# Optimization experiments

Hardware: AMD Instinct MI355X
Metric: run time of the kernel (lower is better)

Reference implementation:

```python
import jax, jax.numpy as jnp
import numpy as np

D_MODEL = 1024
NUM_HEADS = 16
D_K = D_MODEL // NUM_HEADS
THETA = 10000.0
SEQ = 4096
BATCH = 1


def _rope(x, token_positions):
    # x: [b, h, s, d_k]; interleaved even/odd rotation as in the torch module
    kd = jnp.arange(0, D_K, 2, dtype=jnp.float32) / D_K          # [d_k/2]
    angles = token_positions[:, None].astype(jnp.float32) / (THETA ** kd)  # [s, d_k/2]
    cos_pos = jnp.cos(angles)
    sin_pos = jnp.sin(angles)
    x_even = x[..., 0::2]
    x_odd = x[..., 1::2]
    rot_even = x_even * cos_pos - x_odd * sin_pos
    rot_odd = x_even * sin_pos + x_odd * cos_pos
    rot = jnp.stack([rot_even, rot_odd], axis=-1)                # [..., d_k/2, 2]
    return rot.reshape(*x.shape[:-1], D_K)


def setup_inputs() -> dict:
    key = jax.random.key(0)
    k1, k2, k3 = jax.random.split(key, 3)
    std_qkv = np.sqrt(2.0 / (D_MODEL + 3 * D_MODEL))
    std_o = np.sqrt(2.0 / (D_MODEL + D_MODEL))
    x = jax.random.normal(k1, (BATCH, SEQ, D_MODEL), dtype=jnp.float32)
    Wqkv = jax.random.normal(k2, (3 * D_MODEL, D_MODEL), dtype=jnp.float32) * std_qkv
    Wo = jax.random.normal(k3, (D_MODEL, D_MODEL), dtype=jnp.float32) * std_o
    token_positions = jnp.arange(SEQ, dtype=jnp.int32)
    return {"x": x, "Wqkv": Wqkv, "Wo": Wo, "token_positions": token_positions}


def reference(x, Wqkv, Wo, token_positions):
    b, s, _ = x.shape
    qkv = jnp.einsum('bsd,ed->bse', x, Wqkv)                      # [b, s, 3*d_model]
    q, k, v = jnp.split(qkv, 3, axis=-1)

    def to_heads(t):
        return t.reshape(b, s, NUM_HEADS, D_K).transpose(0, 2, 1, 3)  # [b, h, s, d_k]

    q, k, v = to_heads(q), to_heads(k), to_heads(v)
    q = _rope(q, token_positions)
    k = _rope(k, token_positions)

    scores = jnp.einsum('bhqd,bhkd->bhqk', q, k) / jnp.sqrt(jnp.float32(D_K))
    mask = jnp.tril(jnp.ones((s, s), dtype=bool))
    scores = jnp.where(mask, scores, -jnp.inf)
    attn = jax.nn.softmax(scores, axis=-1)
    out = jnp.einsum('bhqk,bhkd->bhqd', attn, v)                  # [b, h, s, d_k]
    out = out.transpose(0, 2, 1, 3).reshape(b, s, D_MODEL)
    return jnp.einsum('bsd,ed->bse', out, Wo)
```

## Files before the change

kernel.cpp:

```cpp
#include <hip/hip_runtime.h>
#include <cstdint>

typedef unsigned short u16;
typedef __attribute__((ext_vector_type(8))) short short8;
typedef __attribute__((ext_vector_type(4))) float float4v;

__device__ __forceinline__ float bf2f(u16 u) {
    union { unsigned int i; float f; } v; v.i = ((unsigned int)u) << 16; return v.f;
}
__device__ __forceinline__ u16 f2bf(float f) {
    union { float f; unsigned int i; } v; v.f = f;
    unsigned int i = v.i;
    i += 0x7fffu + ((i >> 16) & 1u);
    return (u16)(i >> 16);
}
__device__ __forceinline__ unsigned cvt_pk_bf16(float lo, float hi) {
    unsigned r;
    asm("v_cvt_pk_bf16_f32 %0, %1, %2" : "=v"(r) : "v"(lo), "v"(hi));
    return r;
}
__device__ __forceinline__ void gl2lds16(const u16* g, u16* l) {
    __builtin_amdgcn_global_load_lds((const __attribute__((address_space(1))) void*)g,
                                     (__attribute__((address_space(3))) void*)l, 16, 0, 0);
}
__device__ __forceinline__ uint4 cvt8(const float* __restrict__ p) {
    float4 a = *(const float4*)p;
    float4 b = *(const float4*)(p + 4);
    u16 t[8] = {f2bf(a.x), f2bf(a.y), f2bf(a.z), f2bf(a.w),
                f2bf(b.x), f2bf(b.y), f2bf(b.z), f2bf(b.w)};
    return *(const uint4*)t;
}

__global__ void cvt_xw(const float* __restrict__ x, const float* __restrict__ wq,
                       const int* __restrict__ pos,
                       u16* __restrict__ xb, u16* __restrict__ wqb,
                       float2* __restrict__ tb) {
    int i = blockIdx.x * blockDim.x + threadIdx.x;
    if (i < 524288) {
        *(uint4*)(xb + (size_t)i * 8) = cvt8(x + (size_t)i * 8);
    } else if (i < 917504) {
        int j = i - 524288;
        *(uint4*)(wqb + (size_t)j * 8) = cvt8(wq + (size_t)j * 8);
    } else {
        int j = i - 917504;
        int s = j >> 5, f = j & 31;
        float freq = __expf(-(float)f * 0.2878231366242557f);
        float ang  = (float)pos[s] * freq;
        float sn, cs;
        __sincosf(ang, &sn, &cs);
        float2 t; t.x = cs; t.y = sn;
        tb[j] = t;
    }
}

__global__ __launch_bounds__(256) void gemm_qkv(const u16* __restrict__ A,
                                                const u16* __restrict__ B,
                                                u16* __restrict__ C,
                                                const float2* __restrict__ tb) {
    __shared__ u16 As[128 * 32];
    __shared__ u16 Bs[128 * 32];
    const int tid  = threadIdx.x;
    const int wave = tid >> 6, lane = tid & 63;
    const int lg = lane >> 4, lr = lane & 15;
    const int bm = blockIdx.x * 128, bn = blockIdx.y * 128;
    const int wm = (wave & 1) * 64, wn = (wave >> 1) * 64;
    const int row = tid >> 2, co = (tid & 3) * 8;

    float4v acc[4][4] = {};

    for (int k0 = 0; k0 < 1024; k0 += 32) {
        gl2lds16(A + (size_t)(bm + row) * 1024 + k0 + co,      As + tid * 8);
        gl2lds16(A + (size_t)(bm + 64 + row) * 1024 + k0 + co, As + (tid + 256) * 8);
        gl2lds16(B + (size_t)(bn + row) * 1024 + k0 + co,      Bs + tid * 8);
        gl2lds16(B + (size_t)(bn + 64 + row) * 1024 + k0 + co, Bs + (tid + 256) * 8);
        __syncthreads();

        short8 af[4], bf[4];
        #pragma unroll
        for (int i = 0; i < 4; ++i)
            af[i] = *(const short8*)(As + (wm + i * 16 + lr) * 32 + lg * 8);
        #pragma unroll
        for (int j = 0; j < 4; ++j)
            bf[j] = *(const short8*)(Bs + (wn + j * 16 + lr) * 32 + lg * 8);
        #pragma unroll
        for (int i = 0; i < 4; ++i)
            #pragma unroll
            for (int j = 0; j < 4; ++j)
                acc[i][j] = __builtin_amdgcn_mfma_f32_16x16x32_bf16(af[i], bf[j], acc[i][j], 0, 0, 0);
        __syncthreads();
    }

    const int colbase = bn + wn;
    const bool dorope = colbase < 2048;
    const float qsc = (colbase < 1024) ? 0.18033688011112042f : 1.0f;
    #pragma unroll
    for (int i = 0; i < 4; ++i)
        #pragma unroll
        for (int r = 0; r < 4; ++r) {
            const int rw = bm + wm + i * 16 + lg * 4 + r;
            #pragma unroll
            for (int j = 0; j < 4; ++j) {
                float v = acc[i][j][r];
                if (dorope) {
                    float2 t = tb[rw * 32 + ((j * 16 + lr) >> 1)];
                    float p = __shfl_xor(v, 1);
                    float rot = (lr & 1) ? (p * t.y + v * t.x)
                                         : (v * t.x - p * t.y);
                    v = rot * qsc;
                }
                C[(size_t)rw * 3072 + colbase + j * 16 + lr] = f2bf(v);
            }
        }
}

__global__ __launch_bounds__(256) void prep2(const u16* __restrict__ qkv,
                                             u16* __restrict__ VT,
                                             float* __restrict__ acc,
                                             float* __restrict__ lac,
                                             const float* __restrict__ wo,
                                             u16* __restrict__ wob) {
    __shared__ u16 T[64 * 65];
    const int bid = blockIdx.x;
    const int tid = threadIdx.x;
    if (bid < 1024) {
        const int h = bid >> 6, s0 = (bid & 63) * 64;
        #pragma unroll
        for (int i = 0; i < 2; ++i) {
            int seg = i * 256 + tid;
            int r = seg >> 3, c8 = (seg & 7) * 8;
            u16 tmp[8];
            *(uint4*)tmp = *(const uint4*)(qkv + (size_t)(s0 + r) * 3072 + 2048 + h * 64 + c8);
            #pragma unroll
            for (int j = 0; j < 8; ++j) T[r * 65 + c8 + j] = tmp[j];
        }
        __syncthreads();
        #pragma unroll
        for (int i = 0; i < 2; ++i) {
            int seg = i * 256 + tid;
            int d = seg >> 3, s8 = (seg & 7) * 8;
            u16 tmp[8];
            #pragma unroll
            for (int j = 0; j < 8; ++j) tmp[j] = T[(s8 + j) * 65 + d];
            *(uint4*)(VT + (size_t)(h * 64 + d) * 4096 + s0 + s8) = *(const uint4*)tmp;
        }
    } else {
        int i = (bid - 1024) * 256 + tid;
        float4 z = {0.f, 0.f, 0.f, 0.f};
        if (i < 1048576) {
            *(float4*)(acc + (size_t)i * 4) = z;
        } else if (i < 1064960) {
            *(float4*)(lac + (size_t)(i - 1048576) * 4) = z;
        } else {
            int j = i - 1064960;
            *(uint4*)(wob + (size_t)j * 8) = cvt8(wo + (size_t)j * 8);
        }
    }
}

__device__ __forceinline__ void attn_tile(const u16* __restrict__ Ksub,
                                          const u16* __restrict__ Vsub,
                                          u16* __restrict__ Psw,
                                          int tbase, int qrow0, int q_abs,
                                          int lg, int lr, int swz,
                                          const short8 qf[2], float4v o_acc[4], float& rs) {
    float4v sc[4];
    #pragma unroll
    for (int jt = 0; jt < 4; ++jt) {
        float4v a = {};
        #pragma unroll
        for (int kk = 0; kk < 2; ++kk) {
            short8 kf = *(const short8*)(Ksub + (jt * 16 + lr) * 64 + (((kk * 4 + lg) ^ swz) * 8));
            a = __builtin_amdgcn_mfma_f32_16x16x32_bf16(kf, qf[kk], a, 0, 0, 0);
        }
        sc[jt] = a;
    }
    const bool mk = (tbase + 63 > qrow0);
    #pragma unroll
    for (int jt = 0; jt < 4; ++jt) {
        float e[4];
        #pragma unroll
        for (int r = 0; r < 4; ++r) {
            float s = sc[jt][r];
            if (mk && (tbase + jt * 16 + lg * 4 + r > q_abs)) s = -30000.f;
            e[r] = __builtin_amdgcn_exp2f(fminf(s, 86.562f));
        }
        rs += (e[0] + e[1]) + (e[2] + e[3]);
        uint2 w;
        w.x = cvt_pk_bf16(e[0], e[1]);
        w.y = cvt_pk_bf16(e[2], e[3]);
        *(uint2*)(Psw + lr * 72 + jt * 16 + lg * 4) = w;
    }
    short8 pf[2];
    #pragma unroll
    for (int kk = 0; kk < 2; ++kk)
        pf[kk] = *(const short8*)(Psw + lr * 72 + kk * 32 + lg * 8);
    #pragma unroll
    for (int jd = 0; jd < 4; ++jd) {
        float4v a = o_acc[jd];
        #pragma unroll
        for (int kk = 0; kk < 2; ++kk) {
            short8 vf = *(const short8*)(Vsub + (jd * 16 + lr) * 64 + (((kk * 4 + lg) ^ swz) * 8));
            a = __builtin_amdgcn_mfma_f32_16x16x32_bf16(pf[kk], vf, a, 0, 0, 0);
        }
        o_acc[jd] = a;
    }
}

__global__ __launch_bounds__(512) void attn_kernel(const u16* __restrict__ qkv,
                                                   const u16* __restrict__ VT,
                                                   float* __restrict__ acc,
                                                   float* __restrict__ lac) {
    __shared__ u16 Ks[2 * 64 * 64];
    __shared__ u16 Vt[2 * 64 * 64];
    __shared__ u16 Ps[8][16 * 72];

    const int tid  = threadIdx.x;
    const int wave = tid >> 6, lane = tid & 63;
    const int lg = lane >> 4, lr = lane & 15;

    const int fid = blockIdx.x;
    const int j_  = fid >> 3;
    const int h   = (fid & 7) * 2 + (j_ >> 5);
    const int z   = (j_ >> 4) & 1;
    const int bxv = j_ & 15;

    const int srow = tid >> 3;
    const int sg   = tid & 7;
    const int sco  = sg * 8;
    const int sldso = srow * 64 + ((sg ^ (srow & 7)) * 8);
    const int swz = (lr & 7);

    const u16* Kgbase = qkv + (size_t)srow * 3072 + 1024 + h * 64 + sco;
    const u16* Vgbase = VT + (size_t)(h * 64 + srow) * 4096 + sco;

    #pragma unroll 1
    for (int part = 0; part < 2; ++part) {
        const int qt = part ? (31 - bxv) : bxv;
        const int qb = qt * 128;
        const int qrow0 = qb + wave * 16;
        const int q_abs = qrow0 + lr;
        const int tmax = qb + 64;
        const int t0s  = z * 64;

        short8 qf[2];
        #pragma unroll
        for (int kk = 0; kk < 2; ++kk)
            qf[kk] = *(const short8*)(qkv + (size_t)(qrow0 + lr) * 3072 + h * 64 + kk * 32 + lg * 8);

        float4v o_acc[4] = {};
        float rs = 0.f;

        uint4 rK0 = *(const uint4*)(Kgbase + (size_t)t0s * 3072);
        uint4 rV0 = *(const uint4*)(Vgbase + t0s);
        const bool pB = (t0s + 128 <= tmax);
        uint4 rK1, rV1;
        if (pB) {
            rK1 = *(const uint4*)(Kgbase + (size_t)(t0s + 128) * 3072);
            rV1 = *(const uint4*)(Vgbase + t0s + 128);
        }
        __syncthreads();
        *(uint4*)(Ks + sldso) = rK0;
        *(uint4*)(Vt + sldso) = rV0;
        if (pB) {
            *(uint4*)(Ks + 4096 + sldso) = rK1;
            *(uint4*)(Vt + 4096 + sldso) = rV1;
        }
        __syncthreads();

        for (int t0 = t0s; t0 <= tmax; t0 += 256) {
            const bool hasB  = (t0 + 128 <= tmax);
            const bool hasN  = (t0 + 256 <= tmax);
            const bool hasNB = (t0 + 384 <= tmax);
            if (hasN) {
                rK0 = *(const uint4*)(Kgbase + (size_t)(t0 + 256) * 3072);
                rV0 = *(const uint4*)(Vgbase + t0 + 256);
            }
            if (hasNB) {
                rK1 = *(const uint4*)(Kgbase + (size_t)(t0 + 384) * 3072);
                rV1 = *(const uint4*)(Vgbase + t0 + 384);
            }

            attn_tile(Ks, Vt, Ps[wave], t0, qrow0, q_abs, lg, lr, swz, qf, o_acc, rs);
            if (hasB)
                attn_tile(Ks + 4096, Vt + 4096, Ps[wave], t0 + 128, qrow0, q_abs,
                          lg, lr, swz, qf, o_acc, rs);

            if (hasN) {
                __syncthreads();
                *(uint4*)(Ks + sldso) = rK0;
                *(uint4*)(Vt + sldso) = rV0;
                if (hasNB) {
                    *(uint4*)(Ks + 4096 + sldso) = rK1;
                    *(uint4*)(Vt + 4096 + sldso) = rV1;
                }
                __syncthreads();
            }
        }

        float t = rs;
        t += __shfl_xor(t, 16, 64);
        t += __shfl_xor(t, 32, 64);
        if (lane < 16)
            atomicAdd(&lac[(size_t)(qrow0 + lr) * 16 + h], t);

        #pragma unroll
        for (int jd = 0; jd < 4; ++jd)
            #pragma unroll
            for (int r = 0; r < 4; ++r) {
                int s = qrow0 + lg * 4 + r;
                int d = jd * 16 + lr;
                atomicAdd(&acc[(size_t)s * 1024 + h * 64 + d], o_acc[jd][r]);
            }
    }
}

__global__ void norm_o(const float* __restrict__ acc, const float* __restrict__ lac,
                       u16* __restrict__ qkv) {
    int i = blockIdx.x * blockDim.x + threadIdx.x;
    if (i >= 4096 * 1024 / 8) return;
    int e0 = i * 8;
    int s = e0 >> 10, c = e0 & 1023, h = c >> 6;
    float inv = 1.0f / lac[(size_t)s * 16 + h];
    float4 a = *(const float4*)(acc + e0);
    float4 b = *(const float4*)(acc + e0 + 4);
    u16 t[8] = {f2bf(a.x * inv), f2bf(a.y * inv), f2bf(a.z * inv), f2bf(a.w * inv),
                f2bf(b.x * inv), f2bf(b.y * inv), f2bf(b.z * inv), f2bf(b.w * inv)};
    *(uint4*)(qkv + (size_t)s * 3072 + c) = *(const uint4*)t;
}

__global__ __launch_bounds__(256) void gemm_oproj(const u16* __restrict__ A,
                                                  const u16* __restrict__ B,
                                                  float* __restrict__ C) {
    __shared__ u16 As[128 * 32];
    __shared__ u16 Bs[64 * 32];
    const int tid  = threadIdx.x;
    const int wave = tid >> 6, lane = tid & 63;
    const int lg = lane >> 4, lr = lane & 15;
    const int bm = blockIdx.x * 128, bn = blockIdx.y * 64;
    const int wm = (wave & 1) * 64, wn = (wave >> 1) * 32;
    const int row = tid >> 2, co = (tid & 3) * 8;

    float4v acc[4][2] = {};

    for (int k0 = 0; k0 < 1024; k0 += 32) {
        gl2lds16(A + (size_t)(bm + row) * 3072 + k0 + co,      As + tid * 8);
        gl2lds16(A + (size_t)(bm + 64 + row) * 3072 + k0 + co, As + (tid + 256) * 8);
        if (row < 64)
            gl2lds16(B + (size_t)(bn + row) * 1024 + k0 + co,  Bs + tid * 8);
        __syncthreads();

        short8 af[4], bf[2];
        #pragma unroll
        for (int i = 0; i < 4; ++i)
            af[i] = *(const short8*)(As + (wm + i * 16 + lr) * 32 + lg * 8);
        #pragma unroll
        for (int j = 0; j < 2; ++j)
            bf[j] = *(const short8*)(Bs + (wn + j * 16 + lr) * 32 + lg * 8);
        #pragma unroll
        for (int i = 0; i < 4; ++i)
            #pragma unroll
            for (int j = 0; j < 2; ++j)
                acc[i][j] = __builtin_amdgcn_mfma_f32_16x16x32_bf16(af[i], bf[j], acc[i][j], 0, 0, 0);
        __syncthreads();
    }

    #pragma unroll
    for (int i = 0; i < 4; ++i)
        #pragma unroll
        for (int j = 0; j < 2; ++j)
            #pragma unroll
            for (int r = 0; r < 4; ++r) {
                int rw = bm + wm + i * 16 + lg * 4 + r;
                int cl = bn + wn + j * 16 + lr;
                C[(size_t)rw * 1024 + cl] = acc[i][j][r];
            }
}

__global__ void fill_diag(float* __restrict__ p, size_t n, float mark) {
    size_t i = (size_t)blockIdx.x * blockDim.x + threadIdx.x;
    if (i < n) p[i] = 0.f;
    if (i == 0) p[0] = mark;
}

extern "C" void kernel_launch(void* const* d_in, const int* in_sizes, int n_in,
                              void* d_out, int out_size, void* d_ws, size_t ws_size,
                              hipStream_t stream) {
    int ix = -1, iwq = -1, iwo = -1, ip = -1;
    for (int i = 0; i < n_in; ++i) {
        if      (in_sizes[i] == 4096 * 1024) ix = i;
        else if (in_sizes[i] == 3072 * 1024) iwq = i;
        else if (in_sizes[i] == 1024 * 1024) iwo = i;
        else if (in_sizes[i] == 4096)        ip = i;
    }
    float* out = (float*)d_out;
    const size_t OUT_E = (size_t)4096 * 1024;
    const size_t QKV_E = (size_t)4096 * 3072;
    const size_t NEED  = QKV_E * 2 + (size_t)3072 * 1024 * 2;

    if (ix < 0 || iwq < 0 || iwo < 0 || ip < 0 || out_size != (int)OUT_E) {
        fill_diag<<<(int)((OUT_E + 255) / 256), 256, 0, stream>>>(out, OUT_E, 1000.0f);
        return;
    }
    if (ws_size < NEED) {
        fill_diag<<<(int)((OUT_E + 255) / 256), 256, 0, stream>>>(out, OUT_E, 500.0f);
        return;
    }
    const float* x    = (const float*)d_in[ix];
    const float* Wqkv = (const float*)d_in[iwq];
    const float* Wo   = (const float*)d_in[iwo];
    const int*   pos  = (const int*)d_in[ip];

    u16* qkv   = (u16*)d_ws;
    u16* wq_bf = (u16*)d_ws + QKV_E;
    u16* wo_bf = wq_bf;
    float* lac = (float*)((char*)wq_bf + 2 * 1024 * 1024 + 65536);
    u16* x_bf  = (u16*)d_out;
    u16* VT    = (u16*)d_out + OUT_E;
    float2* tb = (float2*)VT;
    float* acc = (float*)d_in[ix];

    cvt_xw<<<4096, 256, 0, stream>>>(x, Wqkv, pos, x_bf, wq_bf, tb);
    gemm_qkv<<<dim3(32, 24), 256, 0, stream>>>(x_bf, wq_bf, qkv, tb);
    prep2<<<5696, 256, 0, stream>>>(qkv, VT, acc, lac, Wo, wo_bf);
    attn_kernel<<<512, 512, 0, stream>>>(qkv, VT, acc, lac);
    norm_o<<<2048, 256, 0, stream>>>(acc, lac, qkv);
    gemm_oproj<<<dim3(32, 16), 256, 0, stream>>>(qkv, wo_bf, out);
}
```

Before: 240.4 us.

## Fuse attention-output normalization into O-projection GEMM and remap GEMM block order

Removes the separate norm_o kernel. gemm_oproj now reads the fp32 attention accumulator directly, divides it by the per-row/head softmax denominator, converts to bf16 and stores it into LDS in place of the prior bf16 buffer. Both GEMMs also switch to a 1D grid with a swizzled block-to-tile mapping, so consecutive blocks land across the 8 XCDs with better L2 locality. The cost is that the A-operand loads become synchronous register loads plus conversion instead of async global-to-LDS copies, and each A element is read as fp32 several times across the N-tiles.

```diff
diff --git a/kernel.cpp b/kernel.cpp
--- a/kernel.cpp
+++ b/kernel.cpp
@@ -62,7 +62,9 @@
     const int tid  = threadIdx.x;
     const int wave = tid >> 6, lane = tid & 63;
     const int lg = lane >> 4, lr = lane & 15;
-    const int bm = blockIdx.x * 128, bn = blockIdx.y * 128;
+    const int fid = blockIdx.x;
+    const int wg  = (fid & 7) * 96 + (fid >> 3);
+    const int bm = (wg & 31) * 128, bn = (wg >> 5) * 128;
     const int wm = (wave & 1) * 64, wn = (wave >> 1) * 64;
     const int row = tid >> 2, co = (tid & 3) * 8;
 
@@ -314,21 +316,8 @@
     }
 }
 
-__global__ void norm_o(const float* __restrict__ acc, const float* __restrict__ lac,
-                       u16* __restrict__ qkv) {
-    int i = blockIdx.x * blockDim.x + threadIdx.x;
-    if (i >= 4096 * 1024 / 8) return;
-    int e0 = i * 8;
-    int s = e0 >> 10, c = e0 & 1023, h = c >> 6;
-    float inv = 1.0f / lac[(size_t)s * 16 + h];
-    float4 a = *(const float4*)(acc + e0);
-    float4 b = *(const float4*)(acc + e0 + 4);
-    u16 t[8] = {f2bf(a.x * inv), f2bf(a.y * inv), f2bf(a.z * inv), f2bf(a.w * inv),
-                f2bf(b.x * inv), f2bf(b.y * inv), f2bf(b.z * inv), f2bf(b.w * inv)};
-    *(uint4*)(qkv + (size_t)s * 3072 + c) = *(const uint4*)t;
-}
-
-__global__ __launch_bounds__(256) void gemm_oproj(const u16* __restrict__ A,
+__global__ __launch_bounds__(256) void gemm_oproj(const float* __restrict__ Aacc,
+                                                  const float* __restrict__ lac,
                                                   const u16* __restrict__ B,
                                                   float* __restrict__ C) {
     __shared__ u16 As[128 * 32];
@@ -336,17 +325,34 @@
     const int tid  = threadIdx.x;
     const int wave = tid >> 6, lane = tid & 63;
     const int lg = lane >> 4, lr = lane & 15;
-    const int bm = blockIdx.x * 128, bn = blockIdx.y * 64;
+    const int fid = blockIdx.x;
+    const int wg  = (fid & 7) * 64 + (fid >> 3);
+    const int bm = (wg & 31) * 128, bn = (wg >> 5) * 64;
     const int wm = (wave & 1) * 64, wn = (wave >> 1) * 32;
     const int row = tid >> 2, co = (tid & 3) * 8;
 
-    float4v acc[4][2] = {};
+    float4v accv[4][2] = {};
 
     for (int k0 = 0; k0 < 1024; k0 += 32) {
-        gl2lds16(A + (size_t)(bm + row) * 3072 + k0 + co,      As + tid * 8);
-        gl2lds16(A + (size_t)(bm + 64 + row) * 3072 + k0 + co, As + (tid + 256) * 8);
-        if (row < 64)
-            gl2lds16(B + (size_t)(bn + row) * 1024 + k0 + co,  Bs + tid * 8);
+        #pragma unroll
+        for (int half = 0; half < 2; ++half) {
+            const int cid = tid + half * 256;
+            const int ar  = cid >> 2;
+            const int aco = (cid & 3) * 8;
+            const int s   = bm + ar;
+            const int c   = k0 + aco;
+            const float inv = 1.0f / lac[(size_t)s * 16 + (c >> 6)];
+            const float* src = Aacc + (size_t)s * 1024 + c;
+            float4 a0 = *(const float4*)(src);
+            float4 a1 = *(const float4*)(src + 4);
+            uint4 w;
+            w.x = cvt_pk_bf16(a0.x * inv, a0.y * inv);
+            w.y = cvt_pk_bf16(a0.z * inv, a0.w * inv);
+            w.z = cvt_pk_bf16(a1.x * inv, a1.y * inv);
+            w.w = cvt_pk_bf16(a1.z * inv, a1.w * inv);
+            *(uint4*)(As + ar * 32 + aco) = w;
+        }
+        gl2lds16(B + (size_t)(bn + row) * 1024 + k0 + co, Bs + tid * 8);
         __syncthreads();
 
         short8 af[4], bf[2];
@@ -360,7 +366,7 @@
         for (int i = 0; i < 4; ++i)
             #pragma unroll
             for (int j = 0; j < 2; ++j)
-                acc[i][j] = __builtin_amdgcn_mfma_f32_16x16x32_bf16(af[i], bf[j], acc[i][j], 0, 0, 0);
+                accv[i][j] = __builtin_amdgcn_mfma_f32_16x16x32_bf16(af[i], bf[j], accv[i][j], 0, 0, 0);
         __syncthreads();
     }
 
@@ -372,7 +378,7 @@
             for (int r = 0; r < 4; ++r) {
                 int rw = bm + wm + i * 16 + lg * 4 + r;
                 int cl = bn + wn + j * 16 + lr;
-                C[(size_t)rw * 1024 + cl] = acc[i][j][r];
+                C[(size_t)rw * 1024 + cl] = accv[i][j][r];
             }
 }
 
@@ -420,9 +426,8 @@
     float* acc = (float*)d_in[ix];
 
     cvt_xw<<<4096, 256, 0, stream>>>(x, Wqkv, pos, x_bf, wq_bf, tb);
-    gemm_qkv<<<dim3(32, 24), 256, 0, stream>>>(x_bf, wq_bf, qkv, tb);
+    gemm_qkv<<<768, 256, 0, stream>>>(x_bf, wq_bf, qkv, tb);
     prep2<<<5696, 256, 0, stream>>>(qkv, VT, acc, lac, Wo, wo_bf);
     attn_kernel<<<512, 512, 0, stream>>>(qkv, VT, acc, lac);
-    norm_o<<<2048, 256, 0, stream>>>(acc, lac, qkv);
-    gemm_oproj<<<dim3(32, 16), 256, 0, stream>>>(qkv, wo_bf, out);
-}
+    gemm_oproj<<<512, 256, 0, stream>>>(acc, lac, wo_bf, out);
+}
```

After: 268.6 us. +11.7%, slower.
